# Performance work log

Measured on AMD Instinct MI355X. Metric: run time of the kernel, lower is better.

## Reference

```python
import jax, jax.numpy as jnp
import numpy as np

N_NODES = 50000
N_GRAPHS = 250
NODES_PER_GRAPH = 200
EDGES_PER_GRAPH = 3200  # avg degree 16
F_IN = 128
EMB = 128
HID = 128
VOCAB = 1000
N_REL = 8


def setup_inputs() -> dict:
    key = jax.random.key(0)
    ks = jax.random.split(key, 16)

    # message: col 0 = discrete token id (stored as float), col 1 = continuous value
    disc = jax.random.randint(ks[0], (N_GRAPHS,), 0, VOCAB).astype(jnp.float32)
    cont = jax.random.normal(ks[1], (N_GRAPHS,), dtype=jnp.float32)
    message = jnp.stack([disc, cont], axis=1)  # [B, 2]

    x = jax.random.normal(ks[2], (N_NODES, F_IN), dtype=jnp.float32)

    # within-graph edges: local indices + per-graph node offset
    offs = (jnp.arange(N_GRAPHS, dtype=jnp.int64) * NODES_PER_GRAPH)[:, None]
    src = (jax.random.randint(ks[3], (N_GRAPHS, EDGES_PER_GRAPH), 0, NODES_PER_GRAPH) + offs).reshape(-1)
    dst = (jax.random.randint(ks[4], (N_GRAPHS, EDGES_PER_GRAPH), 0, NODES_PER_GRAPH) + offs).reshape(-1)
    edge_index = jnp.stack([src, dst], axis=0).astype(jnp.int64)  # [2, E]
    edge_type = jax.random.randint(ks[5], (N_GRAPHS * EDGES_PER_GRAPH,), 0, N_REL).astype(jnp.int64)

    batch = jnp.repeat(jnp.arange(N_GRAPHS, dtype=jnp.int64), NODES_PER_GRAPH)  # [N]

    s = 0.05
    W1 = jax.random.normal(ks[6], (N_REL, F_IN, EMB), dtype=jnp.float32) * s
    root1 = jax.random.normal(ks[7], (F_IN, EMB), dtype=jnp.float32) * s
    b1 = jnp.zeros((EMB,), dtype=jnp.float32)
    W2 = jax.random.normal(ks[8], (N_REL, EMB, EMB), dtype=jnp.float32) * s
    root2 = jax.random.normal(ks[9], (EMB, EMB), dtype=jnp.float32) * s
    b2 = jnp.zeros((EMB,), dtype=jnp.float32)
    embed_table = jax.random.normal(ks[10], (VOCAB, EMB), dtype=jnp.float32) * s
    cont_w = jax.random.normal(ks[11], (1, EMB), dtype=jnp.float32) * s
    cont_b = jnp.zeros((EMB,), dtype=jnp.float32)
    msg_w = jax.random.normal(ks[12], (2 * EMB, HID), dtype=jnp.float32) * s
    msg_b = jnp.zeros((HID,), dtype=jnp.float32)

    return {
        "message": message, "x": x, "edge_index": edge_index, "edge_type": edge_type,
        "batch": batch, "max_nodes": NODES_PER_GRAPH,
        "W1": W1, "root1": root1, "b1": b1, "W2": W2, "root2": root2, "b2": b2,
        "embed_table": embed_table, "cont_w": cont_w, "cont_b": cont_b,
        "msg_w": msg_w, "msg_b": msg_b,
    }


def _rgcn_conv(h, src, dst, edge_type, W, root, b, n_nodes, n_rel):
    # per-node per-relation transform, then gather per edge: avoids [E,F,F] weight gather
    hW = jnp.einsum('nf,rfo->nro', h, W)          # [N, R, O]
    msg = hW[src, edge_type]                       # [E, O]
    # mean aggregation per (dst, relation) as in PyG RGCNConv(aggr='mean')
    key_dr = dst * n_rel + edge_type
    cnt = jax.ops.segment_sum(jnp.ones_like(edge_type, dtype=h.dtype), key_dr,
                              num_segments=n_nodes * n_rel)
    norm = 1.0 / jnp.maximum(cnt[key_dr], 1.0)     # [E]
    agg = jax.ops.segment_sum(msg * norm[:, None], dst, num_segments=n_nodes)  # [N, O]
    return agg + h @ root + b


def reference(message, x, edge_index, edge_type, batch, max_nodes,
              W1, root1, b1, W2, root2, b2,
              embed_table, cont_w, cont_b, msg_w, msg_b):
    n_nodes = x.shape[0]
    n_rel = W1.shape[0]
    n_graphs = message.shape[0]
    src, dst = edge_index[0], edge_index[1]

    # --- RGCN node embeddings (2 layers, ReLU between) ---
    h = _rgcn_conv(x, src, dst, edge_type, W1, root1, b1, n_nodes, n_rel)
    h = jax.nn.relu(h)
    node_emb = _rgcn_conv(h, src, dst, edge_type, W2, root2, b2, n_nodes, n_rel)  # [N, EMB]

    # --- message representation ---
    disc_tok = message[:, 0].astype(jnp.int32)
    disc_emb = embed_table[disc_tok]                                   # [B, EMB]
    cont_emb = jax.nn.relu(message[:, 1:2] @ cont_w + cont_b)          # [B, EMB]
    combined = jnp.concatenate([disc_emb, cont_emb], axis=1)           # [B, 2*EMB]
    message_repr = jax.nn.relu(combined @ msg_w + msg_b)               # [B, HID]

    # --- per-node dot score against its graph's message, padded per graph ---
    scores = jnp.einsum('ne,ne->n', node_emb, message_repr[batch])     # [N]
    counts = jax.ops.segment_sum(jnp.ones((n_nodes,), dtype=jnp.int32), batch,
                                 num_segments=n_graphs)
    start = jnp.cumsum(counts) - counts                                # exclusive cumsum
    pos = jnp.arange(n_nodes) - start[batch]                           # slot within graph
    logits = jnp.full((n_graphs, max_nodes), -jnp.inf, dtype=scores.dtype)
    logits = logits.at[batch, pos].set(scores)
    return logits
```

## Files before the change

### kernel.cpp

```cpp
#include <hip/hip_runtime.h>
#include <stdint.h>

#define G_   250
#define P_   200
#define EPG  3200
#define E_   800000
#define F_   128
#define R_   8
#define HROW 136
#define NKEY (R_ * P_)

typedef _Float16 f16x8 __attribute__((ext_vector_type(8)));
typedef _Float16 f16x4 __attribute__((ext_vector_type(4)));
typedef float    f32x4 __attribute__((ext_vector_type(4)));

__global__ __launch_bounds__(256) void k_wstage(const float* __restrict__ W1, const float* __restrict__ root1,
                                                const float* __restrict__ W2, const float* __restrict__ root2,
                                                _Float16* __restrict__ wf) {
  int t = blockIdx.x * 256 + threadIdx.x;
  if (t >= 2 * 9 * 8 * 4 * 64 * 8) return;
  int j = t & 7;
  int rest = t >> 3;
  int lane = rest & 63; rest >>= 6;
  int kt = rest & 3;    rest >>= 2;
  int nt = rest & 7;    rest >>= 3;
  int r = rest % 9;
  int l = rest / 9;
  int k = kt * 32 + (lane >> 4) * 8 + j;
  int n = nt * 16 + (lane & 15);
  const float* Wl = (l == 0) ? W1 : W2;
  const float* rl = (l == 0) ? root1 : root2;
  float v = (r < 8) ? Wl[(r * F_ + k) * F_ + n] : rl[k * F_ + n];
  wf[t] = (_Float16)v;
}

__global__ __launch_bounds__(512) void k_main(
    const float* __restrict__ x, const int* __restrict__ ei, const int* __restrict__ et,
    const _Float16* __restrict__ wf, const float* __restrict__ b1, const float* __restrict__ b2,
    const float* __restrict__ message, const float* __restrict__ embed,
    const float* __restrict__ cw, const float* __restrict__ cb,
    const float* __restrict__ mw, const float* __restrict__ mb,
    float* __restrict__ out) {
  __shared__ __attribute__((aligned(16))) _Float16 hbuf[P_ * HROW];
  __shared__ unsigned short csrS[EPG];
  __shared__ int offsS[NKEY + 1];
  __shared__ float msgS[F_ + 1];
  __shared__ float scoreS[2 * P_];
  __shared__ int cnt[NKEY];
  __shared__ int cur[NKEY];
  __shared__ int chunkTot[200];
  __shared__ int scanA[256];
  __shared__ int scanB[256];
  __shared__ int eRec[EPG];
  __shared__ float comb[256];
  __shared__ float red[512];

  int g = blockIdx.x, tid = threadIdx.x;
  int lane = tid & 63, wave = tid >> 6, quad = lane >> 4, lc = lane & 15;

  for (int i = tid; i < P_ * 32; i += 512) {
    int row = i >> 5, c4 = i & 31;
    const float4 v = ((const float4*)x)[(g * P_ + row) * 32 + c4];
    f16x4 pk = { (_Float16)v.x, (_Float16)v.y, (_Float16)v.z, (_Float16)v.w };
    *((f16x4*)&hbuf[row * HROW + c4 * 4]) = pk;
  }
  for (int i = tid; i < NKEY; i += 512) { cnt[i] = 0; cur[i] = 0; }
  if (tid < F_) {
    int tok = (int)message[g * 2];
    float cont = message[g * 2 + 1];
    comb[tid] = embed[tok * F_ + tid];
    float ce = cont * cw[tid] + cb[tid];
    comb[F_ + tid] = ce > 0.0f ? ce : 0.0f;
  }
  __syncthreads();
  int base = g * EPG, nbase = g * P_;
  for (int e = tid; e < EPG; e += 512) {
    int s = ei[base + e] - nbase;
    int d = ei[E_ + base + e] - nbase;
    int r = et[base + e];
    eRec[e] = s | (d << 8) | (r << 16);
    atomicAdd(&cnt[r * P_ + d], 1);
  }
  __syncthreads();
  if (tid < 200) {
    int s = 0;
    for (int i = 0; i < 8; i++) { int c = cnt[tid * 8 + i]; offsS[tid * 8 + i] = s; s += c; }
    chunkTot[tid] = s;
    scanA[tid] = s;
  }
  __syncthreads();
  {
    int* src = scanA; int* dst = scanB;
    for (int st = 1; st < 256; st <<= 1) {
      if (tid < 200) dst[tid] = src[tid] + (tid >= st ? src[tid - st] : 0);
      __syncthreads();
      int* tmp = src; src = dst; dst = tmp;
    }
  }
  if (tid < 200) {
    int add = scanA[tid] - chunkTot[tid];
    for (int i = 0; i < 8; i++) offsS[tid * 8 + i] += add;
  }
  if (tid == 0) offsS[NKEY] = EPG;
  {
    int col = tid & 127, seg = tid >> 7;
    float acc = 0.0f;
#pragma unroll 8
    for (int k = seg * 64; k < seg * 64 + 64; k++) acc += comb[k] * mw[k * F_ + col];
    red[tid] = acc;
  }
  __syncthreads();
  for (int e = tid; e < EPG; e += 512) {
    int rec = eRec[e];
    int s = rec & 255, d = (rec >> 8) & 255, r = rec >> 16;
    int key = r * P_ + d;
    int pos = atomicAdd(&cur[key], 1);
    csrS[offsS[key] + pos] = (unsigned short)s;
  }
  if (tid < F_) {
    float a = mb[tid] + red[tid] + red[128 + tid] + red[256 + tid] + red[384 + tid];
    a = a > 0.0f ? a : 0.0f;
    msgS[tid] = a;
    comb[tid] = a * b2[tid];
  }
  __syncthreads();
  if (tid < 64) comb[tid] += comb[tid + 64];
  __syncthreads();
  if (tid < 32) comb[tid] += comb[tid + 32];
  __syncthreads();
  if (tid < 16) comb[tid] += comb[tid + 16];
  __syncthreads();
  if (tid == 0) {
    float s = 0.0f;
    for (int i = 0; i < 16; i++) s += comb[i];
    msgS[F_] = s;
  }
  __syncthreads();

  int mgrp = wave >> 1, ngrp = wave & 1;
  int myD = lc;
  int cq = quad * 8;

  for (int l = 0; l < 2; l++) {
    f32x4 acc[4][4];
#pragma unroll
    for (int a = 0; a < 4; a++)
#pragma unroll
      for (int b = 0; b < 4; b++) acc[a][b] = f32x4{0.0f, 0.0f, 0.0f, 0.0f};
    const _Float16* wl = wf + l * (9 * 8 * 4 * 64 * 8);
    for (int r = 0; r < 9; r++) {
      f16x8 Bf[4][4];
      const _Float16* wr = wl + r * (8 * 4 * 64 * 8);
#pragma unroll
      for (int ntj = 0; ntj < 4; ntj++)
#pragma unroll
        for (int kt = 0; kt < 4; kt++)
          Bf[ntj][kt] = *((const f16x8*)(wr + (((ngrp * 4 + ntj) * 4 + kt) * 64 + lane) * 8));
#pragma unroll
      for (int mtj = 0; mtj < 4; mtj++) {
        int mt = mgrp + mtj * 4;
        if (mt < 13) {
          f16x8 a0, a1, a2, a3;
          if (r < 8) {
            int d = mt * 16 + myD;
            int o = 0, n = 0;
            if (d < P_) { int key = r * P_ + d; o = offsS[key]; n = offsS[key + 1] - o; }
            a0 = f16x8{0,0,0,0,0,0,0,0}; a1 = a0; a2 = a0; a3 = a0;
            int sNext = (n > 0) ? (int)csrS[o] : 0;
            for (int t = 0; t < n; t++) {
              int sc = sNext;
              if (t + 1 < n) sNext = (int)csrS[o + t + 1];
              const _Float16* hp = &hbuf[sc * HROW + cq];
              a0 += *((const f16x8*)(hp));
              a1 += *((const f16x8*)(hp + 32));
              a2 += *((const f16x8*)(hp + 64));
              a3 += *((const f16x8*)(hp + 96));
            }
            float nf = (n > 0) ? 1.0f / (float)n : 0.0f;
            _Float16 nh = (_Float16)nf;
            a0 *= nh; a1 *= nh; a2 *= nh; a3 *= nh;
          } else {
            int rowA = mt * 16 + myD; rowA = rowA < P_ ? rowA : P_ - 1;
            const _Float16* hp = &hbuf[rowA * HROW + cq];
            a0 = *((const f16x8*)(hp));
            a1 = *((const f16x8*)(hp + 32));
            a2 = *((const f16x8*)(hp + 64));
            a3 = *((const f16x8*)(hp + 96));
          }
#pragma unroll
          for (int ntj = 0; ntj < 4; ntj++) {
            acc[mtj][ntj] = __builtin_amdgcn_mfma_f32_16x16x32_f16(a0, Bf[ntj][0], acc[mtj][ntj], 0, 0, 0);
            acc[mtj][ntj] = __builtin_amdgcn_mfma_f32_16x16x32_f16(a1, Bf[ntj][1], acc[mtj][ntj], 0, 0, 0);
            acc[mtj][ntj] = __builtin_amdgcn_mfma_f32_16x16x32_f16(a2, Bf[ntj][2], acc[mtj][ntj], 0, 0, 0);
            acc[mtj][ntj] = __builtin_amdgcn_mfma_f32_16x16x32_f16(a3, Bf[ntj][3], acc[mtj][ntj], 0, 0, 0);
          }
        }
      }
    }
    __syncthreads();
    if (l == 0) {
#pragma unroll
      for (int mtj = 0; mtj < 4; mtj++) {
        int mt = mgrp + mtj * 4;
        if (mt < 13) {
#pragma unroll
          for (int ntj = 0; ntj < 4; ntj++) {
            int col = (ngrp * 4 + ntj) * 16 + lc;
            float bias = b1[col];
#pragma unroll
            for (int reg = 0; reg < 4; reg++) {
              int row = mt * 16 + quad * 4 + reg;
              float v = acc[mtj][ntj][reg] + bias;
              v = v > 0.0f ? v : 0.0f;
              if (row < P_) hbuf[row * HROW + col] = (_Float16)v;
            }
          }
        }
      }
      __syncthreads();
    } else {
#pragma unroll
      for (int mtj = 0; mtj < 4; mtj++) {
        int mt = mgrp + mtj * 4;
        if (mt < 13) {
#pragma unroll
          for (int reg = 0; reg < 4; reg++) {
            float p = 0.0f;
#pragma unroll
            for (int ntj = 0; ntj < 4; ntj++)
              p += acc[mtj][ntj][reg] * msgS[(ngrp * 4 + ntj) * 16 + lc];
            p += __shfl_xor(p, 8, 16);
            p += __shfl_xor(p, 4, 16);
            p += __shfl_xor(p, 2, 16);
            p += __shfl_xor(p, 1, 16);
            int row = mt * 16 + quad * 4 + reg;
            if (lc == 0 && row < P_) scoreS[ngrp * P_ + row] = p;
          }
        }
      }
      __syncthreads();
      for (int i = tid; i < P_; i += 512)
        out[g * P_ + i] = scoreS[i] + scoreS[P_ + i] + msgS[F_];
    }
  }
}

extern "C" void kernel_launch(void* const* d_in, const int* in_sizes, int n_in,
                              void* d_out, int out_size, void* d_ws, size_t ws_size,
                              hipStream_t stream) {
  const float* message = (const float*)d_in[0];
  const float* x       = (const float*)d_in[1];
  const int*   ei      = (const int*)d_in[2];
  const int*   et      = (const int*)d_in[3];
  const float* W1      = (const float*)d_in[6];
  const float* root1   = (const float*)d_in[7];
  const float* b1      = (const float*)d_in[8];
  const float* W2      = (const float*)d_in[9];
  const float* root2   = (const float*)d_in[10];
  const float* b2      = (const float*)d_in[11];
  const float* embed   = (const float*)d_in[12];
  const float* cw      = (const float*)d_in[13];
  const float* cb      = (const float*)d_in[14];
  const float* mw      = (const float*)d_in[15];
  const float* mb      = (const float*)d_in[16];

  _Float16* wfrag = (_Float16*)d_ws;
  float*    out   = (float*)d_out;

  hipLaunchKernelGGL(k_wstage, dim3(1152), dim3(256), 0, stream, W1, root1, W2, root2, wfrag);
  hipLaunchKernelGGL(k_main, dim3(G_), dim3(512), 0, stream, x, ei, et, wfrag, b1, b2,
                     message, embed, cw, cb, mw, mb, out);
}
```

Measured before the change: 189.2 us.

## Switch RGCN matmul to 32x32x16 MFMA with per-wave row ownership

Replaces the 16x16x32 MFMA tiling, where each wave covered a 16-row tile group across half the output columns, with 32x32x16 MFMA. Each of the 8 waves now owns 25 destination rows across all 128 columns, so every neighbour gather is done once per row instead of once per column-half. Layer 1 output goes to a second LDS buffer that aliases the scratch arrays, which removes a barrier and the score staging buffer, and launch bounds now request 2 blocks per CU. The cost is 7 of 32 MMA rows wasted per wave, more B-fragment registers (32 f16x8 per relation), and higher LDS use that may conflict with the occupancy hint.

```diff
diff --git a/kernel.cpp b/kernel.cpp
--- a/kernel.cpp
+++ b/kernel.cpp
@@ -13,6 +13,7 @@
 typedef _Float16 f16x8 __attribute__((ext_vector_type(8)));
 typedef _Float16 f16x4 __attribute__((ext_vector_type(4)));
 typedef float    f32x4 __attribute__((ext_vector_type(4)));
+typedef float    f32x16 __attribute__((ext_vector_type(16)));
 
 __global__ __launch_bounds__(256) void k_wstage(const float* __restrict__ W1, const float* __restrict__ root1,
                                                 const float* __restrict__ W2, const float* __restrict__ root2,
@@ -22,47 +23,50 @@
   int j = t & 7;
   int rest = t >> 3;
   int lane = rest & 63; rest >>= 6;
-  int kt = rest & 3;    rest >>= 2;
-  int nt = rest & 7;    rest >>= 3;
+  int ntj = rest & 3;   rest >>= 2;
+  int kt = rest & 7;    rest >>= 3;
   int r = rest % 9;
   int l = rest / 9;
-  int k = kt * 32 + (lane >> 4) * 8 + j;
-  int n = nt * 16 + (lane & 15);
+  int k = kt * 16 + (lane >> 5) * 8 + j;
+  int n = ntj * 32 + (lane & 31);
   const float* Wl = (l == 0) ? W1 : W2;
   const float* rl = (l == 0) ? root1 : root2;
   float v = (r < 8) ? Wl[(r * F_ + k) * F_ + n] : rl[k * F_ + n];
   wf[t] = (_Float16)v;
 }
 
-__global__ __launch_bounds__(512) void k_main(
+__global__ __launch_bounds__(512, 2) void k_main(
     const float* __restrict__ x, const int* __restrict__ ei, const int* __restrict__ et,
     const _Float16* __restrict__ wf, const float* __restrict__ b1, const float* __restrict__ b2,
     const float* __restrict__ message, const float* __restrict__ embed,
     const float* __restrict__ cw, const float* __restrict__ cb,
     const float* __restrict__ mw, const float* __restrict__ mb,
     float* __restrict__ out) {
-  __shared__ __attribute__((aligned(16))) _Float16 hbuf[P_ * HROW];
+  __shared__ __attribute__((aligned(16))) _Float16 hbuf0[P_ * HROW];
+  __shared__ __attribute__((aligned(16))) _Float16 hbuf1[P_ * HROW];
   __shared__ unsigned short csrS[EPG];
   __shared__ int offsS[NKEY + 1];
   __shared__ float msgS[F_ + 1];
-  __shared__ float scoreS[2 * P_];
-  __shared__ int cnt[NKEY];
-  __shared__ int cur[NKEY];
-  __shared__ int chunkTot[200];
-  __shared__ int scanA[256];
-  __shared__ int scanB[256];
-  __shared__ int eRec[EPG];
-  __shared__ float comb[256];
-  __shared__ float red[512];
 
   int g = blockIdx.x, tid = threadIdx.x;
-  int lane = tid & 63, wave = tid >> 6, quad = lane >> 4, lc = lane & 15;
+  int lane = tid & 63, wave = tid >> 6;
+  int m32 = lane & 31, kh = lane >> 5;
+
+  int*   Sint     = (int*)hbuf1;
+  int*   cnt      = Sint;
+  int*   cur      = Sint + 1600;
+  int*   chunkTot = Sint + 3200;
+  int*   scanA    = Sint + 3400;
+  int*   scanB    = Sint + 3656;
+  float* comb     = (float*)(Sint + 3912);
+  float* red      = comb + 256;
+  int*   eRec     = (int*)(red + 512);
 
   for (int i = tid; i < P_ * 32; i += 512) {
     int row = i >> 5, c4 = i & 31;
     const float4 v = ((const float4*)x)[(g * P_ + row) * 32 + c4];
     f16x4 pk = { (_Float16)v.x, (_Float16)v.y, (_Float16)v.z, (_Float16)v.w };
-    *((f16x4*)&hbuf[row * HROW + c4 * 4]) = pk;
+    *((f16x4*)&hbuf0[row * HROW + c4 * 4]) = pk;
   }
   for (int i = tid; i < NKEY; i += 512) { cnt[i] = 0; cur[i] = 0; }
   if (tid < F_) {
@@ -137,110 +141,91 @@
   }
   __syncthreads();
 
-  int mgrp = wave >> 1, ngrp = wave & 1;
-  int myD = lc;
-  int cq = quad * 8;
+  int jobBase = wave * 25;
+  bool rowAct = (m32 < 25);
+  int myD = jobBase + m32;
+  int ck = kh * 8;
 
   for (int l = 0; l < 2; l++) {
-    f32x4 acc[4][4];
-#pragma unroll
-    for (int a = 0; a < 4; a++)
-#pragma unroll
-      for (int b = 0; b < 4; b++) acc[a][b] = f32x4{0.0f, 0.0f, 0.0f, 0.0f};
+    const _Float16* Ap = (l == 0) ? hbuf0 : hbuf1;
+    f32x16 acc[4];
+#pragma unroll
+    for (int nt = 0; nt < 4; nt++)
+#pragma unroll
+      for (int i = 0; i < 16; i++) acc[nt][i] = 0.0f;
     const _Float16* wl = wf + l * (9 * 8 * 4 * 64 * 8);
     for (int r = 0; r < 9; r++) {
-      f16x8 Bf[4][4];
+      f16x8 Bf[8][4];
       const _Float16* wr = wl + r * (8 * 4 * 64 * 8);
 #pragma unroll
-      for (int ntj = 0; ntj < 4; ntj++)
-#pragma unroll
-        for (int kt = 0; kt < 4; kt++)
-          Bf[ntj][kt] = *((const f16x8*)(wr + (((ngrp * 4 + ntj) * 4 + kt) * 64 + lane) * 8));
-#pragma unroll
-      for (int mtj = 0; mtj < 4; mtj++) {
-        int mt = mgrp + mtj * 4;
-        if (mt < 13) {
-          f16x8 a0, a1, a2, a3;
-          if (r < 8) {
-            int d = mt * 16 + myD;
-            int o = 0, n = 0;
-            if (d < P_) { int key = r * P_ + d; o = offsS[key]; n = offsS[key + 1] - o; }
-            a0 = f16x8{0,0,0,0,0,0,0,0}; a1 = a0; a2 = a0; a3 = a0;
-            int sNext = (n > 0) ? (int)csrS[o] : 0;
-            for (int t = 0; t < n; t++) {
-              int sc = sNext;
-              if (t + 1 < n) sNext = (int)csrS[o + t + 1];
-              const _Float16* hp = &hbuf[sc * HROW + cq];
-              a0 += *((const f16x8*)(hp));
-              a1 += *((const f16x8*)(hp + 32));
-              a2 += *((const f16x8*)(hp + 64));
-              a3 += *((const f16x8*)(hp + 96));
-            }
-            float nf = (n > 0) ? 1.0f / (float)n : 0.0f;
-            _Float16 nh = (_Float16)nf;
-            a0 *= nh; a1 *= nh; a2 *= nh; a3 *= nh;
-          } else {
-            int rowA = mt * 16 + myD; rowA = rowA < P_ ? rowA : P_ - 1;
-            const _Float16* hp = &hbuf[rowA * HROW + cq];
-            a0 = *((const f16x8*)(hp));
-            a1 = *((const f16x8*)(hp + 32));
-            a2 = *((const f16x8*)(hp + 64));
-            a3 = *((const f16x8*)(hp + 96));
-          }
-#pragma unroll
-          for (int ntj = 0; ntj < 4; ntj++) {
-            acc[mtj][ntj] = __builtin_amdgcn_mfma_f32_16x16x32_f16(a0, Bf[ntj][0], acc[mtj][ntj], 0, 0, 0);
-            acc[mtj][ntj] = __builtin_amdgcn_mfma_f32_16x16x32_f16(a1, Bf[ntj][1], acc[mtj][ntj], 0, 0, 0);
-            acc[mtj][ntj] = __builtin_amdgcn_mfma_f32_16x16x32_f16(a2, Bf[ntj][2], acc[mtj][ntj], 0, 0, 0);
-            acc[mtj][ntj] = __builtin_amdgcn_mfma_f32_16x16x32_f16(a3, Bf[ntj][3], acc[mtj][ntj], 0, 0, 0);
-          }
+      for (int kt = 0; kt < 8; kt++)
+#pragma unroll
+        for (int nt = 0; nt < 4; nt++)
+          Bf[kt][nt] = *((const f16x8*)(wr + ((kt * 4 + nt) * 64 + lane) * 8));
+      f16x8 a[8];
+      if (r < 8) {
+        int o = 0, n = 0;
+        if (rowAct) { int key = r * P_ + myD; o = offsS[key]; n = offsS[key + 1] - o; }
+        f16x8 z = {0, 0, 0, 0, 0, 0, 0, 0};
+#pragma unroll
+        for (int kt = 0; kt < 8; kt++) a[kt] = z;
+        int sNext = (n > 0) ? (int)csrS[o] : 0;
+        for (int t = 0; t < n; t++) {
+          int sc = sNext;
+          if (t + 1 < n) sNext = (int)csrS[o + t + 1];
+          const _Float16* hp = &Ap[sc * HROW + ck];
+#pragma unroll
+          for (int kt = 0; kt < 8; kt++) a[kt] += *((const f16x8*)(hp + kt * 16));
         }
+        float nf = (n > 0) ? 1.0f / (float)n : 0.0f;
+        _Float16 nh = (_Float16)nf;
+#pragma unroll
+        for (int kt = 0; kt < 8; kt++) a[kt] *= nh;
+      } else {
+        int rowA = jobBase + (rowAct ? m32 : 24);
+        const _Float16* hp = &Ap[rowA * HROW + ck];
+#pragma unroll
+        for (int kt = 0; kt < 8; kt++) a[kt] = *((const f16x8*)(hp + kt * 16));
       }
+#pragma unroll
+      for (int kt = 0; kt < 8; kt++)
+#pragma unroll
+        for (int nt = 0; nt < 4; nt++)
+          acc[nt] = __builtin_amdgcn_mfma_f32_32x32x16_f16(a[kt], Bf[kt][nt], acc[nt], 0, 0, 0);
     }
-    __syncthreads();
     if (l == 0) {
 #pragma unroll
-      for (int mtj = 0; mtj < 4; mtj++) {
-        int mt = mgrp + mtj * 4;
-        if (mt < 13) {
-#pragma unroll
-          for (int ntj = 0; ntj < 4; ntj++) {
-            int col = (ngrp * 4 + ntj) * 16 + lc;
-            float bias = b1[col];
-#pragma unroll
-            for (int reg = 0; reg < 4; reg++) {
-              int row = mt * 16 + quad * 4 + reg;
-              float v = acc[mtj][ntj][reg] + bias;
-              v = v > 0.0f ? v : 0.0f;
-              if (row < P_) hbuf[row * HROW + col] = (_Float16)v;
-            }
+      for (int nt = 0; nt < 4; nt++) {
+        int col = nt * 32 + m32;
+        float bias = b1[col];
+#pragma unroll
+        for (int reg = 0; reg < 16; reg++) {
+          int row = (reg & 3) + 8 * (reg >> 2) + 4 * kh;
+          if (row < 25) {
+            float v = acc[nt][reg] + bias;
+            v = v > 0.0f ? v : 0.0f;
+            hbuf1[(jobBase + row) * HROW + col] = (_Float16)v;
           }
         }
       }
       __syncthreads();
     } else {
-#pragma unroll
-      for (int mtj = 0; mtj < 4; mtj++) {
-        int mt = mgrp + mtj * 4;
-        if (mt < 13) {
-#pragma unroll
-          for (int reg = 0; reg < 4; reg++) {
-            float p = 0.0f;
-#pragma unroll
-            for (int ntj = 0; ntj < 4; ntj++)
-              p += acc[mtj][ntj][reg] * msgS[(ngrp * 4 + ntj) * 16 + lc];
-            p += __shfl_xor(p, 8, 16);
-            p += __shfl_xor(p, 4, 16);
-            p += __shfl_xor(p, 2, 16);
-            p += __shfl_xor(p, 1, 16);
-            int row = mt * 16 + quad * 4 + reg;
-            if (lc == 0 && row < P_) scoreS[ngrp * P_ + row] = p;
-          }
-        }
+      float db2 = msgS[F_];
+#pragma unroll
+      for (int reg = 0; reg < 16; reg++) {
+        int row = (reg & 3) + 8 * (reg >> 2) + 4 * kh;
+        float p = 0.0f;
+#pragma unroll
+        for (int nt = 0; nt < 4; nt++)
+          p += acc[nt][reg] * msgS[nt * 32 + m32];
+        p += __shfl_xor(p, 16, 32);
+        p += __shfl_xor(p, 8, 32);
+        p += __shfl_xor(p, 4, 32);
+        p += __shfl_xor(p, 2, 32);
+        p += __shfl_xor(p, 1, 32);
+        if (m32 == 0 && row < 25)
+          out[g * P_ + jobBase + row] = p + db2;
       }
-      __syncthreads();
-      for (int i = tid; i < P_; i += 512)
-        out[g * P_ + i] = scoreS[i] + scoreS[P_ + i] + msgS[F_];
     }
   }
 }
```

After: 189.7 us. No clear change (+0.3%).
